# Performance work log

Measured on AMD Instinct MI355X. Metric: run time of the kernel, lower is better.

Reference implementation:

```python
import jax, jax.numpy as jnp
import numpy as np

N_NODES = 100000


def setup_inputs() -> dict:
    key = jax.random.key(0)
    k1, k2, k3, k4, k5, k6 = jax.random.split(key, 6)
    N, E, F_IN, F_OUT = N_NODES, 1600000, 128, 128
    stdv = 1.0 / np.sqrt(F_OUT)
    return {
        "input_features": jax.random.normal(k1, (N, F_IN), dtype=jnp.float32),
        "edge_row": jnp.sort(jax.random.randint(k2, (E,), 0, N, dtype=jnp.int32)),
        "edge_col": jax.random.randint(k3, (E,), 0, N, dtype=jnp.int32),
        "edge_val": jax.random.uniform(k4, (E,), dtype=jnp.float32),
        "weight": jax.random.uniform(k5, (F_IN, F_OUT), minval=-stdv, maxval=stdv, dtype=jnp.float32),
        "bias": jax.random.uniform(k6, (F_OUT,), minval=-stdv, maxval=stdv, dtype=jnp.float32),
    }


def reference(input_features, edge_row, edge_col, edge_val, weight, bias):
    # support = X @ W   [N, F_out]  (dense GEMM)
    support = jnp.matmul(input_features, weight)
    # output = spmm(adj, support): COO adjacency, segment-sum over destination rows
    msgs = edge_val[:, None] * support[edge_col]          # [E, F_out] gather
    output = jax.ops.segment_sum(msgs, edge_row, num_segments=N_NODES)
    return output + bias
```

## Files before the change

### kernel.cpp

```cpp
#include <hip/hip_runtime.h>

typedef unsigned int uint;
typedef unsigned short ushort;
typedef unsigned char uchar;
typedef unsigned long long ull;
typedef __attribute__((ext_vector_type(4))) float f32x4;
typedef __attribute__((ext_vector_type(2))) float f32x2;
typedef __attribute__((ext_vector_type(4))) uint u32x4;
typedef __attribute__((ext_vector_type(2))) uint u32x2;

#define NNODES 100000
#define NPAD   100032
#define NEDGES 1600000
#define FD 128
#define BM 64
#define RPW 8

__device__ __forceinline__ uint cvt_pk_bf16(float lo, float hi) {
    uint r;
    asm("v_cvt_pk_bf16_f32 %0, %1, %2" : "=v"(r) : "v"(lo), "v"(hi));
    return r;
}
__device__ __forceinline__ int swz(int row, int k) {
    return (row * 256 + k * 2) ^ ((row & 7) << 4);
}

__global__ __launch_bounds__(256) void prep(const float* __restrict__ W,
                                            ushort* __restrict__ Wt,
                                            const int* __restrict__ rows,
                                            int* __restrict__ ptr) {
    const int bid = blockIdx.x;
    if (bid < 16) {
        const int sid = bid * 256 + threadIdx.x;
        const int n = sid & 127, k0 = (sid >> 7) * 4;
        const float w0 = W[(k0 + 0) * FD + n];
        const float w1 = W[(k0 + 1) * FD + n];
        const float w2 = W[(k0 + 2) * FD + n];
        const float w3 = W[(k0 + 3) * FD + n];
        u32x2 p;
        p.x = cvt_pk_bf16(w0, w1);
        p.y = cvt_pk_bf16(w2, w3);
        *(u32x2*)((char*)Wt + swz(n, k0)) = p;
    } else {
        const int r = (bid - 16) * 256 + threadIdx.x;
        if (r > NNODES) return;
        int lo = 0, hi = NEDGES;
        while (lo < hi) {
            const int mid = (lo + hi) >> 1;
            const bool lt = rows[mid] < r;
            lo = lt ? mid + 1 : lo;
            hi = lt ? hi : mid;
        }
        ptr[r] = lo;
    }
}

__global__ __launch_bounds__(256) void gemm_mfma_q8(const float* __restrict__ X,
                                                    const ushort* __restrict__ Wt,
                                                    uchar* __restrict__ S8,
                                                    float* __restrict__ scale) {
    __shared__ ushort As[BM * FD];
    __shared__ ushort Bs[FD * FD];
    const int tid = threadIdx.x;
    const int row0 = blockIdx.x * BM;

    #pragma unroll
    for (int it = 0; it < 8; ++it) {
        const int idx = tid + it * 256;
        const int r = idx >> 5, k0 = (idx & 31) * 4;
        const int grow = min(row0 + r, NNODES - 1);
        const float4 g = *(const float4*)&X[grow * FD + k0];
        u32x2 p;
        p.x = cvt_pk_bf16(g.x, g.y);
        p.y = cvt_pk_bf16(g.z, g.w);
        *(u32x2*)((char*)As + swz(r, k0)) = p;
    }
    #pragma unroll
    for (int it = 0; it < 8; ++it) {
        const int b = (tid + it * 256) * 16;
        *(u32x4*)((char*)Bs + b) = *(const u32x4*)((const char*)Wt + b);
    }
    __syncthreads();

    const int lane = tid & 63, wv = tid >> 6;
    const int l15 = lane & 15, kg = lane >> 4;
    const int arow = wv * 16 + l15;

    f32x4 acc[8];
    #pragma unroll
    for (int i = 0; i < 8; ++i) acc[i] = (f32x4)0.f;

    #pragma unroll
    for (int ks = 0; ks < 4; ++ks) {
        const int k0 = ks * 32 + kg * 8;
        const u32x4 a = *(const u32x4*)((const char*)As + swz(arow, k0));
        #pragma unroll
        for (int nf = 0; nf < 8; ++nf) {
            const u32x4 b = *(const u32x4*)((const char*)Bs + swz(nf * 16 + l15, k0));
            asm volatile("v_mfma_f32_16x16x32_bf16 %0, %1, %2, %0"
                         : "+v"(acc[nf]) : "v"(a), "v"(b));
        }
    }
    asm volatile("s_nop 7\ns_nop 7\ns_nop 7");

    __syncthreads();
    uchar* As8 = (uchar*)As;

    #pragma unroll
    for (int r = 0; r < 4; ++r) {
        float m = 0.f;
        #pragma unroll
        for (int nf = 0; nf < 8; ++nf) m = fmaxf(m, fabsf(acc[nf][r]));
        m = fmaxf(m, __shfl_xor(m, 1));
        m = fmaxf(m, __shfl_xor(m, 2));
        m = fmaxf(m, __shfl_xor(m, 4));
        m = fmaxf(m, __shfl_xor(m, 8));
        m = fmaxf(m, 1e-20f);
        const int lrow = wv * 16 + kg * 4 + r;
        if (l15 == 0) scale[row0 + lrow] = m * (1.f / 127.f);
        const float inv = 127.f / m;
        #pragma unroll
        for (int nf = 0; nf < 8; ++nf) {
            const int q = (int)rintf(acc[nf][r] * inv) + 128;
            As8[lrow * FD + nf * 16 + l15] = (uchar)q;
        }
    }
    __syncthreads();
    #pragma unroll
    for (int it = 0; it < 2; ++it) {
        const int o = (tid + it * 256) * 16;
        *(u32x4*)(S8 + (size_t)row0 * FD + o) = *(const u32x4*)(As8 + o);
    }
}

__global__ __launch_bounds__(256) void build_vs(const int* __restrict__ ecol,
                                                const float* __restrict__ eval_,
                                                const float* __restrict__ scale,
                                                float* __restrict__ VS) {
    const int i = blockIdx.x * 256 + threadIdx.x;
    if (i < NEDGES) VS[i] = eval_[i] * scale[ecol[i]];
}

__global__ __launch_bounds__(256, 8) void spmm16(const int* __restrict__ rptr,
                                                 const int* __restrict__ erow,
                                                 const int* __restrict__ ecol,
                                                 const float* __restrict__ VS,
                                                 const uchar* __restrict__ S8,
                                                 const float* __restrict__ bias,
                                                 float* __restrict__ out) {
    const int wv = (blockIdx.x * 256 + threadIdx.x) >> 6;
    const int lane = threadIdx.x & 63;
    const int r0 = wv * RPW;
    const f32x2 b2 = *(const f32x2*)&bias[lane * 2];
    const uint voff = (uint)lane << 1;

    const int E0 = __builtin_amdgcn_readfirstlane(rptr[r0]);
    const int E1 = __builtin_amdgcn_readfirstlane(rptr[r0 + RPW]);

    const int ml = lane & 15;
    const uint* mb = (lane < 16) ? (const uint*)ecol
                   : (lane < 32) ? (const uint*)VS
                                 : (const uint*)erow;

    float a0 = 0.f, a1 = 0.f, sv = 0.f;

    if (E0 < E1) {
        const int nb = (E1 - E0 + 15) >> 4;
        int rcur = __builtin_amdgcn_readfirstlane(erow[E0]);

#define LOADMETA(M_, b_) { \
        const int i_ = min(E0 + (b_) * 16 + ml, NEDGES - 1); \
        M_ = __builtin_nontemporal_load(&mb[i_]); }

#define GATHER(G_, M_) { \
        _Pragma("unroll") for (int j = 0; j < 16; ++j) { \
            const uint c_ = (uint)__builtin_amdgcn_readlane((int)(M_), j); \
            G_[j] = (uint)*(const ushort*)(S8 + ((size_t)c_ << 7) + voff); } }

#define FLUSH() { f32x2 o_; \
        o_.x = fmaf(-128.f, sv, a0) + b2.x; \
        o_.y = fmaf(-128.f, sv, a1) + b2.y; \
        __builtin_nontemporal_store(o_, (f32x2*)&out[(size_t)rcur * FD + voff]); \
        a0 = 0.f; a1 = 0.f; sv = 0.f; }

#define EDGE(gj, M_, j) { \
        const int rj = __builtin_amdgcn_readlane((int)(M_), 32 + j); \
        const float vj = __int_as_float(__builtin_amdgcn_readlane((int)(M_), 16 + j)); \
        if (rj != rcur) { FLUSH(); rcur = rj; } \
        a0 = fmaf(vj, (float)(gj & 0xffu), a0); \
        a1 = fmaf(vj, (float)(gj >> 8), a1); \
        sv += vj; }

#define PROC(G_, M_) { \
        _Pragma("unroll") for (int j = 0; j < 16; ++j) { EDGE(G_[j], M_, j) } }

#define PROC_LAST(G_, M_, b_) { \
        _Pragma("unroll") for (int j = 0; j < 16; ++j) { \
            if (E0 + (b_) * 16 + j < E1) { EDGE(G_[j], M_, j) } } }

#define STEP(GC, GN, MC, MN, ML, b_) { \
        if ((b_) + 1 < nb) GATHER(GN, MN); \
        if ((b_) + 2 < nb) LOADMETA(ML, (b_) + 2); \
        if ((b_) == nb - 1) { PROC_LAST(GC, MC, b_) } else { PROC(GC, MC) } }

        uint mA, mB = 0, mC = 0;
        uint gA[16], gB[16];

        LOADMETA(mA, 0);
        LOADMETA(mB, 1);
        GATHER(gA, mA);

        int b = 0;
        while (true) {
            STEP(gA, gB, mA, mB, mC, b); if (++b >= nb) break;
            STEP(gB, gA, mB, mC, mA, b); if (++b >= nb) break;
            STEP(gA, gB, mC, mA, mB, b); if (++b >= nb) break;
            STEP(gB, gA, mA, mB, mC, b); if (++b >= nb) break;
            STEP(gA, gB, mB, mC, mA, b); if (++b >= nb) break;
            STEP(gB, gA, mC, mA, mB, b); if (++b >= nb) break;
        }
        FLUSH();

#undef STEP
#undef PROC_LAST
#undef PROC
#undef EDGE
#undef FLUSH
#undef GATHER
#undef LOADMETA
    }

    const int rl = r0 + ((lane < RPW) ? lane : RPW - 1);
    const bool em = (lane < RPW) && (rptr[rl] == rptr[rl + 1]);
    ull mask = __ballot(em);
    while (mask) {
        const int i = __ffsll(mask) - 1;
        mask &= mask - 1;
        __builtin_nontemporal_store(b2, (f32x2*)&out[(size_t)(r0 + i) * FD + voff]);
    }
}

extern "C" void kernel_launch(void* const* d_in, const int* in_sizes, int n_in,
                              void* d_out, int out_size, void* d_ws, size_t ws_size,
                              hipStream_t stream) {
    const float* X    = (const float*)d_in[0];
    const int*   erow = (const int*)d_in[1];
    const int*   ecol = (const int*)d_in[2];
    const float* eval_= (const float*)d_in[3];
    const float* W    = (const float*)d_in[4];
    const float* bias = (const float*)d_in[5];
    float* out = (float*)d_out;

    uchar* S8    = (uchar*)d_ws;
    float* scale = (float*)((char*)d_ws + 13u * 1024 * 1024);
    int*   rpt   = (int*)((char*)d_ws + 14u * 1024 * 1024);
    float* VS    = (float*)((char*)d_ws + 15u * 1024 * 1024);
    ushort* Wt   = (ushort*)((char*)d_ws + 22u * 1024 * 1024);

    prep<<<16 + (NNODES + 256) / 256, 256, 0, stream>>>(W, Wt, erow, rpt);
    gemm_mfma_q8<<<NPAD / BM, 256, 0, stream>>>(X, Wt, S8, scale);
    build_vs<<<(NEDGES + 255) / 256, 256, 0, stream>>>(ecol, eval_, scale, VS);
    spmm16<<<NNODES / RPW / 4, 256, 0, stream>>>(rpt, erow, ecol, VS, S8, bias, out);
}
```

Baseline: 97.08 us.

## Restructure SpMM into 8-edge batches with uniform-row fast path and deeper prefetch

The SpMM kernel now processes edges in batches of 8 instead of 16 and prefetches metadata three batches ahead. Edge values and first/last row ids are pulled out via readlane before processing. When a whole batch belongs to one row, a fast path skips the per-edge row comparisons. Rows per wave rise from 8 to 10, and nontemporal loads and stores become regular ones. The aim is less scalar per-edge overhead and more gathers in flight, at the cost of smaller batches and different cache behaviour for the output writes.

```diff
diff --git a/kernel.cpp b/kernel.cpp
--- a/kernel.cpp
+++ b/kernel.cpp
@@ -5,7 +5,6 @@
 typedef unsigned char uchar;
 typedef unsigned long long ull;
 typedef __attribute__((ext_vector_type(4))) float f32x4;
-typedef __attribute__((ext_vector_type(2))) float f32x2;
 typedef __attribute__((ext_vector_type(4))) uint u32x4;
 typedef __attribute__((ext_vector_type(2))) uint u32x2;
 
@@ -14,7 +13,7 @@
 #define NEDGES 1600000
 #define FD 128
 #define BM 64
-#define RPW 8
+#define RPW 10
 
 __device__ __forceinline__ uint cvt_pk_bf16(float lo, float hi) {
     uint r;
@@ -141,7 +140,7 @@
     if (i < NEDGES) VS[i] = eval_[i] * scale[ecol[i]];
 }
 
-__global__ __launch_bounds__(256, 8) void spmm16(const int* __restrict__ rptr,
+__global__ __launch_bounds__(256, 8) void spmm_u(const int* __restrict__ rptr,
                                                  const int* __restrict__ erow,
                                                  const int* __restrict__ ecol,
                                                  const float* __restrict__ VS,
@@ -151,92 +150,116 @@
     const int wv = (blockIdx.x * 256 + threadIdx.x) >> 6;
     const int lane = threadIdx.x & 63;
     const int r0 = wv * RPW;
-    const f32x2 b2 = *(const f32x2*)&bias[lane * 2];
+    const float2 b2 = *(const float2*)&bias[lane * 2];
     const uint voff = (uint)lane << 1;
 
     const int E0 = __builtin_amdgcn_readfirstlane(rptr[r0]);
     const int E1 = __builtin_amdgcn_readfirstlane(rptr[r0 + RPW]);
 
-    const int ml = lane & 15;
-    const uint* mb = (lane < 16) ? (const uint*)ecol
-                   : (lane < 32) ? (const uint*)VS
+    const int sl = lane & 7;
+    const uint* mb = (lane < 8) ? (const uint*)ecol
+                   : (lane < 16) ? (const uint*)VS
                                  : (const uint*)erow;
 
     float a0 = 0.f, a1 = 0.f, sv = 0.f;
 
     if (E0 < E1) {
-        const int nb = (E1 - E0 + 15) >> 4;
+        const int nb = (E1 - E0 + 7) >> 3;
         int rcur = __builtin_amdgcn_readfirstlane(erow[E0]);
 
 #define LOADMETA(M_, b_) { \
-        const int i_ = min(E0 + (b_) * 16 + ml, NEDGES - 1); \
-        M_ = __builtin_nontemporal_load(&mb[i_]); }
+        const int i_ = min(E0 + (b_) * 8 + sl, NEDGES - 1); \
+        M_ = mb[i_]; }
 
 #define GATHER(G_, M_) { \
-        _Pragma("unroll") for (int j = 0; j < 16; ++j) { \
+        _Pragma("unroll") for (int j = 0; j < 8; ++j) { \
             const uint c_ = (uint)__builtin_amdgcn_readlane((int)(M_), j); \
             G_[j] = (uint)*(const ushort*)(S8 + ((size_t)c_ << 7) + voff); } }
 
-#define FLUSH() { f32x2 o_; \
+#define EXTRACT(V_, RF_, RL_, M_) { \
+        _Pragma("unroll") for (int j = 0; j < 8; ++j) \
+            V_[j] = __int_as_float(__builtin_amdgcn_readlane((int)(M_), 8 + j)); \
+        RF_ = __builtin_amdgcn_readlane((int)(M_), 16); \
+        RL_ = __builtin_amdgcn_readlane((int)(M_), 23); }
+
+#define FLUSH() { float2 o_; \
         o_.x = fmaf(-128.f, sv, a0) + b2.x; \
         o_.y = fmaf(-128.f, sv, a1) + b2.y; \
-        __builtin_nontemporal_store(o_, (f32x2*)&out[(size_t)rcur * FD + voff]); \
+        *(float2*)&out[(size_t)rcur * FD + voff] = o_; \
         a0 = 0.f; a1 = 0.f; sv = 0.f; }
 
-#define EDGE(gj, M_, j) { \
-        const int rj = __builtin_amdgcn_readlane((int)(M_), 32 + j); \
-        const float vj = __int_as_float(__builtin_amdgcn_readlane((int)(M_), 16 + j)); \
-        if (rj != rcur) { FLUSH(); rcur = rj; } \
+#define ACC(gj, vj) { \
         a0 = fmaf(vj, (float)(gj & 0xffu), a0); \
         a1 = fmaf(vj, (float)(gj >> 8), a1); \
         sv += vj; }
 
-#define PROC(G_, M_) { \
-        _Pragma("unroll") for (int j = 0; j < 16; ++j) { EDGE(G_[j], M_, j) } }
-
-#define PROC_LAST(G_, M_, b_) { \
-        _Pragma("unroll") for (int j = 0; j < 16; ++j) { \
-            if (E0 + (b_) * 16 + j < E1) { EDGE(G_[j], M_, j) } } }
-
-#define STEP(GC, GN, MC, MN, ML, b_) { \
-        if ((b_) + 1 < nb) GATHER(GN, MN); \
-        if ((b_) + 2 < nb) LOADMETA(ML, (b_) + 2); \
-        if ((b_) == nb - 1) { PROC_LAST(GC, MC, b_) } else { PROC(GC, MC) } }
+#define PROC(G_, V_, RF_, RL_, M_) { \
+        if (RF_ == RL_) {                        \
+            if (RF_ != rcur) { FLUSH(); rcur = RF_; } \
+            _Pragma("unroll") for (int j = 0; j < 8; ++j) ACC(G_[j], V_[j]) \
+        } else {                                 \
+            _Pragma("unroll") for (int j = 0; j < 8; ++j) { \
+                const int rj = (j == 0) ? RF_ : (j == 7) ? RL_ \
+                    : __builtin_amdgcn_readlane((int)(M_), 16 + j); \
+                if (rj != rcur) { FLUSH(); rcur = rj; } \
+                ACC(G_[j], V_[j]) \
+            } \
+        } }
+
+#define PROC_TAIL(G_, V_, RF_, RL_, M_, b_) { \
+        _Pragma("unroll") for (int j = 0; j < 8; ++j) { \
+            if (E0 + (b_) * 8 + j < E1) { \
+                const int rj = (j == 0) ? RF_ \
+                    : __builtin_amdgcn_readlane((int)(M_), 16 + j); \
+                if (rj != rcur) { FLUSH(); rcur = rj; } \
+                ACC(G_[j], V_[j]) \
+            } } }
+
+#define STEP(GC, GN, VC, VN, RFC, RLC, RFN, RLN, MC, MN, b_) { \
+        if ((b_) + 1 < nb) { GATHER(GN, MN); EXTRACT(VN, RFN, RLN, MN); } \
+        if ((b_) == nb - 1) { PROC_TAIL(GC, VC, RFC, RLC, MC, b_) } \
+        else { PROC(GC, VC, RFC, RLC, MC) } \
+        if ((b_) + 3 < nb) LOADMETA(MC, (b_) + 3); }
 
         uint mA, mB = 0, mC = 0;
-        uint gA[16], gB[16];
+        uint gA[8], gB[8];
+        float vA[8], vB[8];
+        int rfA = 0, rlA = 0, rfB = 0, rlB = 0;
 
         LOADMETA(mA, 0);
-        LOADMETA(mB, 1);
+        if (nb > 1) LOADMETA(mB, 1);
+        if (nb > 2) LOADMETA(mC, 2);
         GATHER(gA, mA);
+        EXTRACT(vA, rfA, rlA, mA);
 
         int b = 0;
         while (true) {
-            STEP(gA, gB, mA, mB, mC, b); if (++b >= nb) break;
-            STEP(gB, gA, mB, mC, mA, b); if (++b >= nb) break;
-            STEP(gA, gB, mC, mA, mB, b); if (++b >= nb) break;
-            STEP(gB, gA, mA, mB, mC, b); if (++b >= nb) break;
-            STEP(gA, gB, mB, mC, mA, b); if (++b >= nb) break;
-            STEP(gB, gA, mC, mA, mB, b); if (++b >= nb) break;
+            STEP(gA, gB, vA, vB, rfA, rlA, rfB, rlB, mA, mB, b); if (++b >= nb) break;
+            STEP(gB, gA, vB, vA, rfB, rlB, rfA, rlA, mB, mC, b); if (++b >= nb) break;
+            STEP(gA, gB, vA, vB, rfA, rlA, rfB, rlB, mC, mA, b); if (++b >= nb) break;
+            STEP(gB, gA, vB, vA, rfB, rlB, rfA, rlA, mA, mB, b); if (++b >= nb) break;
+            STEP(gA, gB, vA, vB, rfA, rlA, rfB, rlB, mB, mC, b); if (++b >= nb) break;
+            STEP(gB, gA, vB, vA, rfB, rlB, rfA, rlA, mC, mA, b); if (++b >= nb) break;
         }
         FLUSH();
 
 #undef STEP
-#undef PROC_LAST
+#undef PROC_TAIL
 #undef PROC
-#undef EDGE
+#undef ACC
 #undef FLUSH
+#undef EXTRACT
 #undef GATHER
 #undef LOADMETA
     }
 
-    const int rl = r0 + ((lane < RPW) ? lane : RPW - 1);
-    const bool em = (lane < RPW) && (rptr[rl] == rptr[rl + 1]);
+    const int rl_ = r0 + ((lane < RPW) ? lane : RPW - 1);
+    const bool em = (lane < RPW) && (rptr[rl_] == rptr[rl_ + 1]);
     ull mask = __ballot(em);
     while (mask) {
         const int i = __ffsll(mask) - 1;
         mask &= mask - 1;
-        __builtin_nontemporal_store(b2, (f32x2*)&out[(size_t)(r0 + i) * FD + voff]);
+        *(float2*)&out[(size_t)(r0 + i) * FD + voff] = b2;
     }
 }
 
@@ -260,5 +283,5 @@
     prep<<<16 + (NNODES + 256) / 256, 256, 0, stream>>>(W, Wt, erow, rpt);
     gemm_mfma_q8<<<NPAD / BM, 256, 0, stream>>>(X, Wt, S8, scale);
     build_vs<<<(NEDGES + 255) / 256, 256, 0, stream>>>(ecol, eval_, scale, VS);
-    spmm16<<<NNODES / RPW / 4, 256, 0, stream>>>(rpt, erow, ecol, VS, S8, bias, out);
-}
+    spmm_u<<<NNODES / RPW / 4, 256, 0, stream>>>(rpt, erow, ecol, VS, S8, bias, out);
+}
```

Measured after the change: 86.95 us. 10.4% less time.
